# Performance work log

Hardware: AMD Instinct MI355X
Metric: run time of the kernel (lower is better)

The kernel has to match this reference:

```python
import jax, jax.numpy as jnp
import numpy as np

B, S, IN_F, OUT_F, RANK = 4, 4096, 4096, 4096, 64

def soft_threshold24(w):
    # 2:4 soft-threshold pruning: groups of 4 along last dim; keep top-2 |w|,
    # soft-threshold by t = 3rd-largest |w| in each group: sign(w)*relu(|w|-t).
    g = w.reshape(w.shape[0], -1, 4)
    a = jnp.abs(g)
    t = jnp.sort(a, axis=-1)[..., 1:2]  # 3rd largest = 2nd smallest of 4
    s = jnp.sign(g) * jnp.maximum(a - t, 0.0)
    return s.reshape(w.shape)

def fake_fp8_mm(a, b):
    # simulated fp8 GEMM per fake_fp8_mm: fp16 operands, fp32 accumulate/output
    return jnp.matmul(a.astype(jnp.float16), b.astype(jnp.float16),
                      preferred_element_type=jnp.float32)

def setup_inputs():
    key = jax.random.key(0)
    k1, k2, k3 = jax.random.split(key, 3)
    x = jax.random.normal(k1, (B, S, IN_F), jnp.float32)
    std_a = float(np.sqrt(2.0 / (IN_F + RANK)))   # xavier_normal_
    std_b = float(np.sqrt(2.0 / (OUT_F + RANK)))
    weight_A = jax.random.normal(k2, (IN_F, RANK), jnp.float32) * std_a
    weight_B = jax.random.normal(k3, (OUT_F, RANK), jnp.float32) * std_b
    bias = jnp.zeros((OUT_F,), jnp.float32)
    scale_A = jnp.float32(1.0)
    scale_B = jnp.float32(1.0)
    return {"x": x, "weight_A": weight_A, "weight_B": weight_B,
            "bias": bias, "scale_A": scale_A, "scale_B": scale_B}

def reference(x, weight_A, weight_B, bias, scale_A, scale_B):
    wA = soft_threshold24(weight_A) * scale_A      # [IN, R], 2:4 sparse along R
    wB = soft_threshold24(weight_B) * scale_B      # [OUT, R], 2:4 sparse along R
    xf = x.reshape(-1, x.shape[-1])                # [N, IN]
    x_proj = fake_fp8_mm(xf, wA)                   # [N, R]   == FP8SparseOp(x, wA.T, None)
    out = fake_fp8_mm(x_proj, wB.T) + bias         # [N, OUT] == FP8SparseOp(x_proj, wB, bias)
    return out.reshape(*x.shape[:-1], OUT_F)
```

## Files before the change

kernel.cpp:

```cpp
#include <hip/hip_runtime.h>
#include <hip/hip_cooperative_groups.h>

namespace cg = cooperative_groups;

#define IN_FEAT 4096
#define OUT_FEAT 4096
#define RANK 64
#define NROWS 16384
#define TM 32
#define BT 512
#define KC2 256
#define SXS 264
#define XP_STRIDE 72
#define KC 256
#define WA_STRIDE 264

typedef _Float16 half_t;
typedef _Float16 f16x4 __attribute__((ext_vector_type(4)));
typedef _Float16 f16x8 __attribute__((ext_vector_type(8)));
typedef float f32x4 __attribute__((ext_vector_type(4)));

__device__ __forceinline__ f16x4 thr4(float4 v, float s) {
    float a0 = fabsf(v.x), a1 = fabsf(v.y), a2 = fabsf(v.z), a3 = fabsf(v.w);
    float lo1 = fminf(a0, a1), hi1 = fmaxf(a0, a1);
    float lo2 = fminf(a2, a3), hi2 = fmaxf(a2, a3);
    float t = fminf(fmaxf(lo1, lo2), fminf(hi1, hi2));
    f16x4 r;
    r[0] = (half_t)(copysignf(fmaxf(a0 - t, 0.0f), v.x) * s);
    r[1] = (half_t)(copysignf(fmaxf(a1 - t, 0.0f), v.y) * s);
    r[2] = (half_t)(copysignf(fmaxf(a2 - t, 0.0f), v.z) * s);
    r[3] = (half_t)(copysignf(fmaxf(a3 - t, 0.0f), v.w) * s);
    return r;
}

__device__ __forceinline__ f16x4 cvt4(f32x4 v) {
    f16x4 h;
    h[0] = (half_t)v[0]; h[1] = (half_t)v[1];
    h[2] = (half_t)v[2]; h[3] = (half_t)v[3];
    return h;
}

__global__ __launch_bounds__(BT) void coop_kernel(
    const float* __restrict__ x, const float* __restrict__ wA,
    const float* __restrict__ wB, const float* __restrict__ bias,
    const float* __restrict__ scaleA, const float* __restrict__ scaleB,
    float* __restrict__ out, half_t* __restrict__ wAT, half_t* __restrict__ wBh)
{
    __shared__ __align__(16) half_t xs[2][TM][SXS];
    __shared__ __align__(16) half_t xp[TM][XP_STRIDE];

    int tid = threadIdx.x;
    int bid = blockIdx.x;

    {
        int id = bid * BT + tid;
        if (id < 131072) {
            bool isB = id >= 65536;
            int gid = id & 65535;
            int row = gid >> 4;
            int gq  = gid & 15;
            const float* src = (isB ? wB : wA) + (size_t)row * RANK + gq * 4;
            float s = isB ? scaleB[0] : scaleA[0];
            f16x4 h = thr4(*(const float4*)src, s);
            if (!isB) {
                int c = gq * 4;
                wAT[(size_t)(c + 0) * IN_FEAT + row] = h[0];
                wAT[(size_t)(c + 1) * IN_FEAT + row] = h[1];
                wAT[(size_t)(c + 2) * IN_FEAT + row] = h[2];
                wAT[(size_t)(c + 3) * IN_FEAT + row] = h[3];
            } else {
                *(f16x4*)(wBh + (size_t)row * RANK + gq * 4) = h;
            }
        }
    }
    cg::this_grid().sync();

    int wave = tid >> 6;
    int lane = tid & 63;
    int l16  = lane & 15;
    int g    = lane >> 4;
    int rowbase = bid * TM;
    int stripe  = wave & 1;
    int quad    = wave >> 1;

    int srow = tid >> 4;
    int sseg = tid & 15;
    const float* srcrow = x + (size_t)(rowbase + srow) * IN_FEAT + sseg * 4;

    f32x4 ld0, ld1, ld2, ld3;

    {
        {
            const f32x4* p = (const f32x4*)(srcrow);
            ld0 = p[0]; ld1 = p[16]; ld2 = p[32]; ld3 = p[48];
            half_t* dst = &xs[0][srow][sseg * 4];
            *(f16x4*)(dst +   0) = cvt4(ld0);
            *(f16x4*)(dst +  64) = cvt4(ld1);
            *(f16x4*)(dst + 128) = cvt4(ld2);
            *(f16x4*)(dst + 192) = cvt4(ld3);
        }
        __syncthreads();

        f32x4 acc = {0, 0, 0, 0};
        const half_t* wcol = wAT + (size_t)(quad * 16 + l16) * IN_FEAT;
        const half_t* arow = &xs[0][stripe * 16 + l16][0];
        const int xsstep = TM * SXS;

        for (int c = 0; c < IN_FEAT / KC2; ++c) {
            if (c + 1 < IN_FEAT / KC2) {
                const f32x4* p = (const f32x4*)(srcrow + (c + 1) * KC2);
                ld0 = p[0]; ld1 = p[16]; ld2 = p[32]; ld3 = p[48];
            }
            int kb = c * KC2;
            const half_t* ar = arow + (c & 1) * xsstep;
#pragma unroll
            for (int k8 = 0; k8 < KC2 / 32; ++k8) {
                f16x8 a = *(const f16x8*)(ar + k8 * 32 + 8 * g);
                f16x8 b = *(const f16x8*)(wcol + kb + k8 * 32 + 8 * g);
                acc = __builtin_amdgcn_mfma_f32_16x16x32_f16(a, b, acc, 0, 0, 0);
            }
            if (c + 1 < IN_FEAT / KC2) {
                half_t* dst = &xs[(c + 1) & 1][srow][sseg * 4];
                *(f16x4*)(dst +   0) = cvt4(ld0);
                *(f16x4*)(dst +  64) = cvt4(ld1);
                *(f16x4*)(dst + 128) = cvt4(ld2);
                *(f16x4*)(dst + 192) = cvt4(ld3);
            }
            __syncthreads();
        }

#pragma unroll
        for (int r = 0; r < 4; ++r)
            xp[stripe * 16 + 4 * g + r][quad * 16 + l16] = (half_t)acc[r];
    }
    __syncthreads();

    {
        const half_t* xprow = &xp[stripe * 16 + l16][0];
        f16x8 a0 = *(const f16x8*)(xprow + 8 * g);
        f16x8 a1 = *(const f16x8*)(xprow + 32 + 8 * g);

        int cb0 = quad * (OUT_FEAT / 4);
#pragma unroll 2
        for (int cb = cb0; cb < cb0 + OUT_FEAT / 4; cb += 64) {
#pragma unroll
            for (int f = 0; f < 4; ++f) {
                int col = cb + 16 * f + l16;
                const half_t* wp = wBh + (size_t)col * RANK;
                f16x8 b0 = *(const f16x8*)(wp + 8 * g);
                f16x8 b1 = *(const f16x8*)(wp + 32 + 8 * g);
                f32x4 acc2 = {0, 0, 0, 0};
                acc2 = __builtin_amdgcn_mfma_f32_16x16x32_f16(a0, b0, acc2, 0, 0, 0);
                acc2 = __builtin_amdgcn_mfma_f32_16x16x32_f16(a1, b1, acc2, 0, 0, 0);
                float bv = bias[col];
#pragma unroll
                for (int r = 0; r < 4; ++r)
                    out[(size_t)(rowbase + stripe * 16 + 4 * g + r) * OUT_FEAT + col] = acc2[r] + bv;
            }
        }
    }
}

__global__ __launch_bounds__(256) void fused_kernel(
    const float* __restrict__ x, const float* __restrict__ wA,
    const float* __restrict__ wB, const float* __restrict__ bias,
    const float* __restrict__ scaleA, const float* __restrict__ scaleB,
    float* __restrict__ out)
{
    __shared__ __align__(16) half_t wAsT[RANK][WA_STRIDE];
    __shared__ float xp_part[2][TM][XP_STRIDE];
    __shared__ __align__(16) half_t xp[TM][XP_STRIDE];

    int tid  = threadIdx.x;
    int wave = tid >> 6;
    int lane = tid & 63;
    int l16  = lane & 15;
    int g    = lane >> 4;
    int rowbase = blockIdx.x * TM;
    int stripe  = wave & 1;
    int ks      = wave >> 1;

    float sA = scaleA[0];
    float sB = scaleB[0];

    const float* xrow = x + (size_t)(rowbase + stripe * 16 + l16) * IN_FEAT;
    f32x4 acc[4] = {f32x4{0,0,0,0}, f32x4{0,0,0,0}, f32x4{0,0,0,0}, f32x4{0,0,0,0}};

    for (int chunk = 0; chunk < IN_FEAT / KC; ++chunk) {
        int k0 = chunk * KC;
#pragma unroll
        for (int pp = 0; pp < 2; ++pp) {
            int p = tid + pp * 256;
            int q = p & 15;
            int r = p >> 4;
            f16x8 vc0, vc1, vc2, vc3;
#pragma unroll
            for (int i = 0; i < 8; ++i) {
                float4 v = *(const float4*)(wA + (size_t)(k0 + 8 * r + i) * RANK + 4 * q);
                f16x4 h = thr4(v, sA);
                vc0[i] = h[0]; vc1[i] = h[1]; vc2[i] = h[2]; vc3[i] = h[3];
            }
            *(f16x8*)&wAsT[4 * q + 0][8 * r] = vc0;
            *(f16x8*)&wAsT[4 * q + 1][8 * r] = vc1;
            *(f16x8*)&wAsT[4 * q + 2][8 * r] = vc2;
            *(f16x8*)&wAsT[4 * q + 3][8 * r] = vc3;
        }
        __syncthreads();

#pragma unroll
        for (int it = 0; it < 4; ++it) {
            int kloc = ks * 128 + it * 32;
            float4 xa = *(const float4*)(xrow + k0 + kloc + 8 * g);
            float4 xb = *(const float4*)(xrow + k0 + kloc + 8 * g + 4);
            f16x8 a;
            a[0] = (half_t)xa.x; a[1] = (half_t)xa.y; a[2] = (half_t)xa.z; a[3] = (half_t)xa.w;
            a[4] = (half_t)xb.x; a[5] = (half_t)xb.y; a[6] = (half_t)xb.z; a[7] = (half_t)xb.w;
#pragma unroll
            for (int f = 0; f < 4; ++f) {
                f16x8 b = *(const f16x8*)&wAsT[16 * f + l16][kloc + 8 * g];
                acc[f] = __builtin_amdgcn_mfma_f32_16x16x32_f16(a, b, acc[f], 0, 0, 0);
            }
        }
        __syncthreads();
    }

#pragma unroll
    for (int f = 0; f < 4; ++f)
#pragma unroll
        for (int r = 0; r < 4; ++r)
            xp_part[ks][stripe * 16 + 4 * g + r][16 * f + l16] = acc[f][r];
    __syncthreads();

#pragma unroll
    for (int i = 0; i < (TM * RANK) / 256; ++i) {
        int e = i * 256 + tid;
        int r = e >> 6, c = e & 63;
        xp[r][c] = (half_t)(xp_part[0][r][c] + xp_part[1][r][c]);
    }
    __syncthreads();

    {
        const half_t* xprow = &xp[stripe * 16 + l16][0];
        f16x8 a0 = *(const f16x8*)(xprow + 8 * g);
        f16x8 a1 = *(const f16x8*)(xprow + 32 + 8 * g);

        int cb0 = ks * (OUT_FEAT / 2);
        for (int cb = cb0; cb < cb0 + OUT_FEAT / 2; cb += 16) {
            int col = cb + l16;
            const float* wp = wB + (size_t)col * RANK;
            float4 w00 = *(const float4*)(wp + 8 * g);
            float4 w01 = *(const float4*)(wp + 8 * g + 4);
            float4 w10 = *(const float4*)(wp + 32 + 8 * g);
            float4 w11 = *(const float4*)(wp + 32 + 8 * g + 4);
            f16x4 b00 = thr4(w00, sB), b01 = thr4(w01, sB);
            f16x4 b10 = thr4(w10, sB), b11 = thr4(w11, sB);
            f16x8 b0, b1;
            b0[0]=b00[0]; b0[1]=b00[1]; b0[2]=b00[2]; b0[3]=b00[3];
            b0[4]=b01[0]; b0[5]=b01[1]; b0[6]=b01[2]; b0[7]=b01[3];
            b1[0]=b10[0]; b1[1]=b10[1]; b1[2]=b10[2]; b1[3]=b10[3];
            b1[4]=b11[0]; b1[5]=b11[1]; b1[6]=b11[2]; b1[7]=b11[3];

            f32x4 acc2 = {0, 0, 0, 0};
            acc2 = __builtin_amdgcn_mfma_f32_16x16x32_f16(a0, b0, acc2, 0, 0, 0);
            acc2 = __builtin_amdgcn_mfma_f32_16x16x32_f16(a1, b1, acc2, 0, 0, 0);
            float bv = bias[col];
#pragma unroll
            for (int r = 0; r < 4; ++r)
                out[(size_t)(rowbase + stripe * 16 + 4 * g + r) * OUT_FEAT + col] = acc2[r] + bv;
        }
    }
}

extern "C" void kernel_launch(void* const* d_in, const int* in_sizes, int n_in,
                              void* d_out, int out_size, void* d_ws, size_t ws_size,
                              hipStream_t stream) {
    const float* x      = (const float*)d_in[0];
    const float* wA     = (const float*)d_in[1];
    const float* wB     = (const float*)d_in[2];
    const float* bias   = (const float*)d_in[3];
    const float* scaleA = (const float*)d_in[4];
    const float* scaleB = (const float*)d_in[5];
    float* out = (float*)d_out;

    const size_t WS_NEED = (size_t)RANK * IN_FEAT * 2
                         + (size_t)OUT_FEAT * RANK * 2;

    bool launched = false;
    if (ws_size >= WS_NEED && d_ws != nullptr) {
        half_t* wAT = (half_t*)d_ws;
        half_t* wBh = wAT + (size_t)RANK * IN_FEAT;
        void* args[] = {(void*)&x, (void*)&wA, (void*)&wB, (void*)&bias,
                        (void*)&scaleA, (void*)&scaleB, (void*)&out,
                        (void*)&wAT, (void*)&wBh};
        hipError_t err = hipLaunchCooperativeKernel((void*)coop_kernel,
                                                    dim3(NROWS / TM), dim3(BT),
                                                    args, 0, stream);
        launched = (err == hipSuccess);
    }
    if (!launched) {
        fused_kernel<<<NROWS / TM, 256, 0, stream>>>(x, wA, wB, bias, scaleA, scaleB, out);
    }
}
```

Before: 256.9 us.

## Stage wB tiles in shared memory, prefetch wA fragments, vectorize wA transpose

The second GEMM now stages each 256-column tile of the pruned wB into a double-buffered shared-memory pool that aliases the x staging buffer. The next tile is prefetched into registers while MFMAs run on the current one, replacing direct global loads of wB per wave. The wA prune-and-transpose prologue now has each thread handle 8 rows and write vectorized 16-byte stores instead of scattered 2-byte stores. In the first GEMM, all eight B fragments per chunk are loaded before the MFMA loop. This adds a barrier per output tile and more register pressure.

```diff
diff --git a/kernel.cpp b/kernel.cpp
--- a/kernel.cpp
+++ b/kernel.cpp
@@ -11,6 +11,8 @@
 #define BT 512
 #define KC2 256
 #define SXS 264
+#define CT 256
+#define WBS 72
 #define XP_STRIDE 72
 #define KC 256
 #define WA_STRIDE 264
@@ -46,31 +48,39 @@
     const float* __restrict__ scaleA, const float* __restrict__ scaleB,
     float* __restrict__ out, half_t* __restrict__ wAT, half_t* __restrict__ wBh)
 {
-    __shared__ __align__(16) half_t xs[2][TM][SXS];
+    __shared__ __align__(16) char pool[2 * CT * WBS * 2];
     __shared__ __align__(16) half_t xp[TM][XP_STRIDE];
+
+    half_t (*xs)[TM][SXS]  = (half_t(*)[TM][SXS])pool;
+    half_t (*wbs)[CT][WBS] = (half_t(*)[CT][WBS])pool;
 
     int tid = threadIdx.x;
     int bid = blockIdx.x;
 
     {
         int id = bid * BT + tid;
-        if (id < 131072) {
-            bool isB = id >= 65536;
-            int gid = id & 65535;
-            int row = gid >> 4;
-            int gq  = gid & 15;
-            const float* src = (isB ? wB : wA) + (size_t)row * RANK + gq * 4;
-            float s = isB ? scaleB[0] : scaleA[0];
-            f16x4 h = thr4(*(const float4*)src, s);
-            if (!isB) {
-                int c = gq * 4;
-                wAT[(size_t)(c + 0) * IN_FEAT + row] = h[0];
-                wAT[(size_t)(c + 1) * IN_FEAT + row] = h[1];
-                wAT[(size_t)(c + 2) * IN_FEAT + row] = h[2];
-                wAT[(size_t)(c + 3) * IN_FEAT + row] = h[3];
-            } else {
-                *(f16x4*)(wBh + (size_t)row * RANK + gq * 4) = h;
-            }
+        if (id < 65536) {
+            int row = id >> 4;
+            int gq  = id & 15;
+            float s = scaleB[0];
+            f16x4 h = thr4(*(const float4*)(wB + (size_t)row * RANK + gq * 4), s);
+            *(f16x4*)(wBh + (size_t)row * RANK + gq * 4) = h;
+        } else if (id < 65536 + 8192) {
+            int t2 = id - 65536;
+            int c4 = t2 & 15;
+            int k8 = t2 >> 4;
+            float s = scaleA[0];
+            f16x8 vc0, vc1, vc2, vc3;
+#pragma unroll
+            for (int i = 0; i < 8; ++i) {
+                float4 v = *(const float4*)(wA + (size_t)(k8 * 8 + i) * RANK + c4 * 4);
+                f16x4 h = thr4(v, s);
+                vc0[i] = h[0]; vc1[i] = h[1]; vc2[i] = h[2]; vc3[i] = h[3];
+            }
+            *(f16x8*)(wAT + (size_t)(c4 * 4 + 0) * IN_FEAT + k8 * 8) = vc0;
+            *(f16x8*)(wAT + (size_t)(c4 * 4 + 1) * IN_FEAT + k8 * 8) = vc1;
+            *(f16x8*)(wAT + (size_t)(c4 * 4 + 2) * IN_FEAT + k8 * 8) = vc2;
+            *(f16x8*)(wAT + (size_t)(c4 * 4 + 3) * IN_FEAT + k8 * 8) = vc3;
         }
     }
     cg::this_grid().sync();
@@ -83,21 +93,19 @@
     int stripe  = wave & 1;
     int quad    = wave >> 1;
 
-    int srow = tid >> 4;
-    int sseg = tid & 15;
-    const float* srcrow = x + (size_t)(rowbase + srow) * IN_FEAT + sseg * 4;
-
-    f32x4 ld0, ld1, ld2, ld3;
-
     {
+        int srow = tid >> 4;
+        int sseg = tid & 15;
+        const float* srcrow = x + (size_t)(rowbase + srow) * IN_FEAT + sseg * 4;
+
         {
             const f32x4* p = (const f32x4*)(srcrow);
-            ld0 = p[0]; ld1 = p[16]; ld2 = p[32]; ld3 = p[48];
+            f32x4 a0 = p[0], a1 = p[16], a2 = p[32], a3 = p[48];
             half_t* dst = &xs[0][srow][sseg * 4];
-            *(f16x4*)(dst +   0) = cvt4(ld0);
-            *(f16x4*)(dst +  64) = cvt4(ld1);
-            *(f16x4*)(dst + 128) = cvt4(ld2);
-            *(f16x4*)(dst + 192) = cvt4(ld3);
+            *(f16x4*)(dst +   0) = cvt4(a0);
+            *(f16x4*)(dst +  64) = cvt4(a1);
+            *(f16x4*)(dst + 128) = cvt4(a2);
+            *(f16x4*)(dst + 192) = cvt4(a3);
         }
         __syncthreads();
 
@@ -105,19 +113,23 @@
         const half_t* wcol = wAT + (size_t)(quad * 16 + l16) * IN_FEAT;
         const half_t* arow = &xs[0][stripe * 16 + l16][0];
         const int xsstep = TM * SXS;
+        f32x4 ld0, ld1, ld2, ld3;
 
         for (int c = 0; c < IN_FEAT / KC2; ++c) {
             if (c + 1 < IN_FEAT / KC2) {
                 const f32x4* p = (const f32x4*)(srcrow + (c + 1) * KC2);
                 ld0 = p[0]; ld1 = p[16]; ld2 = p[32]; ld3 = p[48];
             }
-            int kb = c * KC2;
+            f16x8 bfr[8];
+#pragma unroll
+            for (int j = 0; j < 8; ++j)
+                bfr[j] = *(const f16x8*)(wcol + c * KC2 + j * 32 + 8 * g);
+
             const half_t* ar = arow + (c & 1) * xsstep;
 #pragma unroll
-            for (int k8 = 0; k8 < KC2 / 32; ++k8) {
-                f16x8 a = *(const f16x8*)(ar + k8 * 32 + 8 * g);
-                f16x8 b = *(const f16x8*)(wcol + kb + k8 * 32 + 8 * g);
-                acc = __builtin_amdgcn_mfma_f32_16x16x32_f16(a, b, acc, 0, 0, 0);
+            for (int j = 0; j < 8; ++j) {
+                f16x8 a = *(const f16x8*)(ar + j * 32 + 8 * g);
+                acc = __builtin_amdgcn_mfma_f32_16x16x32_f16(a, bfr[j], acc, 0, 0, 0);
             }
             if (c + 1 < IN_FEAT / KC2) {
                 half_t* dst = &xs[(c + 1) & 1][srow][sseg * 4];
@@ -140,23 +152,58 @@
         f16x8 a0 = *(const f16x8*)(xprow + 8 * g);
         f16x8 a1 = *(const f16x8*)(xprow + 32 + 8 * g);
 
-        int cb0 = quad * (OUT_FEAT / 4);
-#pragma unroll 2
-        for (int cb = cb0; cb < cb0 + OUT_FEAT / 4; cb += 64) {
+        int sc = tid >> 1;
+        int sh = tid & 1;
+
+        {
+            const half_t* src = wBh + 0 * (CT * RANK) + (size_t)sc * RANK + sh * 32;
+            f16x8 w0 = *(const f16x8*)(src + 0);
+            f16x8 w1 = *(const f16x8*)(src + 8);
+            f16x8 w2 = *(const f16x8*)(src + 16);
+            f16x8 w3 = *(const f16x8*)(src + 24);
+            half_t* dst = &wbs[0][sc][sh * 32];
+            *(f16x8*)(dst + 0)  = w0;
+            *(f16x8*)(dst + 8)  = w1;
+            *(f16x8*)(dst + 16) = w2;
+            *(f16x8*)(dst + 24) = w3;
+        }
+        __syncthreads();
+
+        for (int ct = 0; ct < OUT_FEAT / CT; ++ct) {
+            f16x8 p0, p1, p2, p3;
+            if (ct + 1 < OUT_FEAT / CT) {
+                const half_t* src = wBh + (size_t)(ct + 1) * (CT * RANK)
+                                  + (size_t)sc * RANK + sh * 32;
+                p0 = *(const f16x8*)(src + 0);
+                p1 = *(const f16x8*)(src + 8);
+                p2 = *(const f16x8*)(src + 16);
+                p3 = *(const f16x8*)(src + 24);
+            }
+
+            const int buf = ct & 1;
 #pragma unroll
             for (int f = 0; f < 4; ++f) {
-                int col = cb + 16 * f + l16;
-                const half_t* wp = wBh + (size_t)col * RANK;
-                f16x8 b0 = *(const f16x8*)(wp + 8 * g);
-                f16x8 b1 = *(const f16x8*)(wp + 32 + 8 * g);
+                int cl = quad * 64 + 16 * f + l16;
+                f16x8 b0 = *(const f16x8*)&wbs[buf][cl][8 * g];
+                f16x8 b1 = *(const f16x8*)&wbs[buf][cl][32 + 8 * g];
                 f32x4 acc2 = {0, 0, 0, 0};
                 acc2 = __builtin_amdgcn_mfma_f32_16x16x32_f16(a0, b0, acc2, 0, 0, 0);
                 acc2 = __builtin_amdgcn_mfma_f32_16x16x32_f16(a1, b1, acc2, 0, 0, 0);
+                int col = ct * CT + cl;
                 float bv = bias[col];
 #pragma unroll
                 for (int r = 0; r < 4; ++r)
                     out[(size_t)(rowbase + stripe * 16 + 4 * g + r) * OUT_FEAT + col] = acc2[r] + bv;
             }
+
+            if (ct + 1 < OUT_FEAT / CT) {
+                half_t* dst = &wbs[(ct + 1) & 1][sc][sh * 32];
+                *(f16x8*)(dst + 0)  = p0;
+                *(f16x8*)(dst + 8)  = p1;
+                *(f16x8*)(dst + 16) = p2;
+                *(f16x8*)(dst + 24) = p3;
+            }
+            __syncthreads();
         }
     }
 }
```

New measurement: 212.1 us. 1.21x faster.
